# Kernel optimization log

Hardware: AMD Instinct MI355X
Metric: run time of the kernel (lower is better)

## Reference

```python
import jax, jax.numpy as jnp
from jax import lax
import numpy as np

# db4 (Daubechies-4) filters, matching pywt.Wavelet('db4')
L = 8
_REC_LO = np.array([0.23037781330885523, 0.7148465705525415, 0.6308807679295904,
                    -0.02798376941698385, -0.18703481171888114, 0.030841381835986965,
                    0.032883011666982945, -0.010597401784997278], dtype=np.float32)
_DEC_LO = _REC_LO[::-1].copy()
_DEC_HI = (((-1.0) ** (np.arange(L) + 1)) * _REC_LO).astype(np.float32)  # QMF
_REC_HI = _DEC_HI[::-1].copy()
# lax.conv performs correlation, so use reversed filters to get true convolution.
# rev(dec_lo)=rec_lo, rev(dec_hi)=rec_hi and vice versa.
DEC_K = jnp.asarray(np.stack([_DEC_LO[::-1], _DEC_HI[::-1]])[:, None, :])  # (2,1,L)
REC_K = jnp.asarray(np.stack([_REC_LO[::-1], _REC_HI[::-1]])[None, :, :])  # (1,2,L)

ENHANCE_FACTOR = 1.5
DENOISE_THRESHOLD = 0.2


def _dwt_last(x):
    # pywt single-level DWT (mode='symmetric') along last axis.
    # Equivalent to: conv(sym_pad(x, L-1), dec_filter)[valid][1::2]
    xe = jnp.pad(x, ((0, 0), (L - 1, L - 1)), mode='symmetric')[:, 1:]
    y = lax.conv_general_dilated(xe[:, None, :], DEC_K, (2,), 'VALID',
                                 dimension_numbers=('NCH', 'OIH', 'NCH'))
    return y[:, 0], y[:, 1]  # lo, hi, each (M, (S+L-1)//2)


def _idwt_last(lo, hi):
    # pywt single-level IDWT: upsample (lhs_dilation=2), filter, trim L-2 each side.
    c = jnp.stack([lo, hi], axis=1)  # (M, 2, n)
    y = lax.conv_general_dilated(c, REC_K, (1,), [(1, 1)], lhs_dilation=(2,),
                                 dimension_numbers=('NCH', 'OIH', 'NCH'))
    return y[:, 0]  # (M, 2n - L + 2)


def _dwt2(x):
    # x: (N, H, W) -> aa (cA), da (cH), ad (cV), dd (cD)
    N, H, W = x.shape
    lo, hi = _dwt_last(x.reshape(N * H, W))
    Wc = lo.shape[-1]
    lo = lo.reshape(N, H, Wc)
    hi = hi.reshape(N, H, Wc)

    def colwise(a):
        at = a.transpose(0, 2, 1).reshape(N * Wc, H)
        l, h = _dwt_last(at)
        Hc = l.shape[-1]
        return (l.reshape(N, Wc, Hc).transpose(0, 2, 1),
                h.reshape(N, Wc, Hc).transpose(0, 2, 1))

    aa, da = colwise(lo)
    ad, dd = colwise(hi)
    return aa, da, ad, dd


def _idwt2(aa, da, ad, dd):
    N, Hc, Wc = aa.shape

    def colinv(a, d):
        at = a.transpose(0, 2, 1).reshape(N * Wc, Hc)
        dt = d.transpose(0, 2, 1).reshape(N * Wc, Hc)
        r = _idwt_last(at, dt)
        H = r.shape[-1]
        return r.reshape(N, Wc, H).transpose(0, 2, 1)

    lo = colinv(aa, da)
    hi = colinv(ad, dd)
    H = lo.shape[1]
    out = _idwt_last(lo.reshape(N * H, Wc), hi.reshape(N * H, Wc))
    return out.reshape(N, H, -1)


def _soft_enhance(d):
    # enhance then pywt.threshold(..., mode='soft') with per-(image,channel,band) max
    d = d * ENHANCE_FACTOR
    t = DENOISE_THRESHOLD * jnp.max(jnp.abs(d), axis=(-2, -1), keepdims=True)
    return jnp.sign(d) * jnp.maximum(jnp.abs(d) - t, 0.0)


def setup_inputs() -> dict:
    key = jax.random.key(0)
    x = jax.random.normal(key, (32, 3, 510, 510), dtype=jnp.float32)
    return {'x': x}


def reference(x):
    B, C, H, W = x.shape
    z = x.reshape(B * C, H, W)
    a1, h1, v1, d1 = _dwt2(z)
    a2, h2, v2, d2 = _dwt2(a1)
    h2s, v2s, d2s = _soft_enhance(h2), _soft_enhance(v2), _soft_enhance(d2)
    h1s, v1s, d1s = _soft_enhance(h1), _soft_enhance(v1), _soft_enhance(d1)
    a1r = _idwt2(a2, h2s, v2s, d2s)
    out = _idwt2(a1r, h1s, v1s, d1s)
    return out.reshape(B, C, H, W)
```

## Files before the change

### kernel.cpp

```cpp
#include <hip/hip_runtime.h>

__constant__ float c_dec_lo[8] = {
    -0.010597401784997278f, 0.032883011666982945f, 0.030841381835986965f,
    -0.18703481171888114f, -0.02798376941698385f, 0.6308807679295904f,
    0.7148465705525415f, 0.23037781330885523f};
__constant__ float c_dec_hi[8] = {
    -0.23037781330885523f, 0.7148465705525415f, -0.6308807679295904f,
    -0.02798376941698385f, 0.18703481171888114f, 0.030841381835986965f,
    -0.032883011666982945f, -0.010597401784997278f};
__constant__ float c_rec_lo[8] = {
    0.23037781330885523f, 0.7148465705525415f, 0.6308807679295904f,
    -0.02798376941698385f, -0.18703481171888114f, 0.030841381835986965f,
    0.032883011666982945f, -0.010597401784997278f};
__constant__ float c_rec_hi[8] = {
    -0.010597401784997278f, -0.032883011666982945f, 0.030841381835986965f,
    0.18703481171888114f, -0.02798376941698385f, -0.6308807679295904f,
    0.7148465705525415f, -0.23037781330885523f};

__device__ __forceinline__ float soft_enh(float v, float th) {
    float e = 1.5f * v;
    float a = fabsf(e) - th;
    return a > 0.0f ? copysignf(a, e) : 0.0f;
}

#define TB 32
#define TO 64

__global__ __launch_bounds__(256, 8) void fused_dwt2_k(
    const float* __restrict__ x, int S, int Nc, int tiles,
    float* __restrict__ aa, float* __restrict__ da,
    float* __restrict__ ad, float* __restrict__ dd,
    unsigned* __restrict__ mx_da, unsigned* __restrict__ mx_ad,
    unsigned* __restrict__ mx_dd)
{
    int b = blockIdx.x;
    int tx = b % tiles, ty = (b / tiles) % tiles, m = b / (tiles * tiles);
    int jh0 = ty * TB, jw0 = tx * TB;
    int r0 = 2 * jh0 - 6, c0 = 2 * jw0 - 6;
    const float* xm = x + (size_t)m * S * S;

    __shared__ float RB[70][65];

    int tid = threadIdx.x;
    bool interior = (r0 >= 0) & (r0 + 69 < S) & (c0 >= 0) & (c0 + 69 < S);

    if (interior) {
        for (int e = tid; e < 70 * 32; e += 256) {
            int r = e >> 5, jj = e & 31;
            const float* row = xm + (size_t)(r0 + r) * S + (c0 + 2 * jj);
            float alo = 0.f, ahi = 0.f;
#pragma unroll
            for (int t = 0; t < 8; ++t) {
                float v = row[7 - t];
                alo = fmaf(c_dec_lo[t], v, alo);
                ahi = fmaf(c_dec_hi[t], v, ahi);
            }
            RB[r][jj] = alo; RB[r][32 + jj] = ahi;
        }
    } else {
        for (int e = tid; e < 70 * 32; e += 256) {
            int r = e >> 5, jj = e & 31;
            int pr = r0 + r;
            pr = pr < 0 ? -1 - pr : pr;
            pr = pr >= S ? 2 * S - 1 - pr : pr;
            const float* row = xm + (size_t)pr * S;
            int pb = c0 + 2 * jj;
            float alo = 0.f, ahi = 0.f;
#pragma unroll
            for (int t = 0; t < 8; ++t) {
                int p = pb + 7 - t;
                p = p < 0 ? -1 - p : p;
                p = p >= S ? 2 * S - 1 - p : p;
                float v = row[p];
                alo = fmaf(c_dec_lo[t], v, alo);
                ahi = fmaf(c_dec_hi[t], v, ahi);
            }
            RB[r][jj] = alo; RB[r][32 + jj] = ahi;
        }
    }
    __syncthreads();

    float mh = 0.f, mv = 0.f, md = 0.f;
    for (int e = tid; e < TB * TB; e += 256) {
        int ii = e >> 5, jj = e & 31;
        float vaa = 0.f, vda = 0.f, vad = 0.f, vdd = 0.f;
#pragma unroll
        for (int t = 0; t < 8; ++t) {
            float l = RB[2 * ii + 7 - t][jj];
            float h = RB[2 * ii + 7 - t][32 + jj];
            vaa = fmaf(c_dec_lo[t], l, vaa);
            vda = fmaf(c_dec_hi[t], l, vda);
            vad = fmaf(c_dec_lo[t], h, vad);
            vdd = fmaf(c_dec_hi[t], h, vdd);
        }
        int jh = jh0 + ii, jw = jw0 + jj;
        if (jh < Nc && jw < Nc) {
            size_t o = ((size_t)m * Nc + jh) * Nc + jw;
            aa[o] = vaa; da[o] = vda; ad[o] = vad; dd[o] = vdd;
            mh = fmaxf(mh, fabsf(vda));
            mv = fmaxf(mv, fabsf(vad));
            md = fmaxf(md, fabsf(vdd));
        }
    }
#pragma unroll
    for (int off = 32; off; off >>= 1) {
        mh = fmaxf(mh, __shfl_down(mh, off));
        mv = fmaxf(mv, __shfl_down(mv, off));
        md = fmaxf(md, __shfl_down(md, off));
    }
    __shared__ float sm[3][4];
    int wv = tid >> 6, ln = tid & 63;
    if (ln == 0) { sm[0][wv] = mh; sm[1][wv] = mv; sm[2][wv] = md; }
    __syncthreads();
    if (tid == 0) {
        float A = fmaxf(fmaxf(sm[0][0], sm[0][1]), fmaxf(sm[0][2], sm[0][3]));
        float B = fmaxf(fmaxf(sm[1][0], sm[1][1]), fmaxf(sm[1][2], sm[1][3]));
        float C = fmaxf(fmaxf(sm[2][0], sm[2][1]), fmaxf(sm[2][2], sm[2][3]));
        atomicMax(mx_da + m, __float_as_uint(A));
        atomicMax(mx_ad + m, __float_as_uint(B));
        atomicMax(mx_dd + m, __float_as_uint(C));
    }
}

__global__ __launch_bounds__(256, 6) void fused_idwt2_k(
    const float* __restrict__ a, const float* __restrict__ h,
    const float* __restrict__ v, const float* __restrict__ d,
    const unsigned* __restrict__ mxh, const unsigned* __restrict__ mxv,
    const unsigned* __restrict__ mxd,
    int n, int Ho, int tiles, float* __restrict__ out)
{
    int b = blockIdx.x;
    int tx = b % tiles, ty = (b / tiles) % tiles, m = b / (tiles * tiles);
    int i0 = ty * TO, u0 = tx * TO;
    int jr0 = i0 >> 1, jc0 = u0 >> 1;

    __shared__ float LH[TO][71];

    int tid = threadIdx.x;
    float th_h = 0.2f * (1.5f * __uint_as_float(mxh[m]));
    float th_v = 0.2f * (1.5f * __uint_as_float(mxv[m]));
    float th_d = 0.2f * (1.5f * __uint_as_float(mxd[m]));
    const float* am = a + (size_t)m * n * n;
    const float* hm = h + (size_t)m * n * n;
    const float* vm = v + (size_t)m * n * n;
    const float* dm = d + (size_t)m * n * n;

    for (int task = tid; task < 8 * 35; task += 256) {
        int g = task / 35, jc = task % 35;
        int jcg = jc0 + jc; if (jcg > n - 1) jcg = n - 1;
        float acc_lo[8], acc_hi[8];
#pragma unroll
        for (int k = 0; k < 8; ++k) { acc_lo[k] = 0.f; acc_hi[k] = 0.f; }
#pragma unroll
        for (int rl = 0; rl < 7; ++rl) {
            int jr = jr0 + 4 * g + rl; if (jr > n - 1) jr = n - 1;
            size_t o = (size_t)jr * n + jcg;
            float av = am[o];
            float hv = soft_enh(hm[o], th_h);
            float vv = soft_enh(vm[o], th_v);
            float dv = soft_enh(dm[o], th_d);
#pragma unroll
            for (int t = 0; t < 8; ++t) {
                int il = 2 * rl + t - 6;
                if (il >= 0 && il < 8) {
                    acc_lo[il] = fmaf(c_rec_lo[t], av, fmaf(c_rec_hi[t], hv, acc_lo[il]));
                    acc_hi[il] = fmaf(c_rec_lo[t], vv, fmaf(c_rec_hi[t], dv, acc_hi[il]));
                }
            }
        }
#pragma unroll
        for (int k = 0; k < 8; ++k) {
            LH[8 * g + k][jc] = acc_lo[k];
            LH[8 * g + k][35 + jc] = acc_hi[k];
        }
    }
    __syncthreads();

    for (int e = tid; e < TO * TO; e += 256) {
        int il = e >> 6, ul = e & 63;
        int t0 = ul & 1;
        float acc = 0.f;
#pragma unroll
        for (int s = 0; s < 4; ++s) {
            int t = t0 + 2 * s;
            int c = (ul + 6 - t) >> 1;
            acc = fmaf(c_rec_lo[t], LH[il][c], acc);
            acc = fmaf(c_rec_hi[t], LH[il][35 + c], acc);
        }
        int gi = i0 + il, gu = u0 + ul;
        if (gi < Ho && gu < Ho)
            out[((size_t)m * Ho + gi) * Ho + gu] = acc;
    }
}

extern "C" void kernel_launch(void* const* d_in, const int* in_sizes, int n_in,
                              void* d_out, int out_size, void* d_ws, size_t ws_size,
                              hipStream_t stream) {
    const float* x = (const float*)d_in[0];
    float* out = (float*)d_out;
    float* ws = (float*)d_ws;

    const int M = 96, S1 = 510, N1 = 258, N2 = 132;
    const long S_l1 = (long)M * N1 * N1;
    const long S_l2 = (long)M * N2 * N2;

    float* aa1 = ws;
    float* h1  = aa1 + S_l1;
    float* v1  = h1 + S_l1;
    float* d1  = v1 + S_l1;
    float* a1r = d1 + S_l1;
    float* a2  = a1r + S_l1;
    float* h2  = a2 + S_l2;
    float* v2  = h2 + S_l2;
    float* d2  = v2 + S_l2;
    unsigned* th = (unsigned*)(d2 + S_l2);

    long need = 5 * S_l1 + 4 * S_l2 + 576;
    if (ws_size < (size_t)need * sizeof(float)) return;

    unsigned *th_h1 = th, *th_v1 = th + 96, *th_d1 = th + 192;
    unsigned *th_h2 = th + 288, *th_v2 = th + 384, *th_d2 = th + 480;

    hipMemsetAsync(th, 0, 576 * sizeof(unsigned), stream);

    fused_dwt2_k<<<9 * 9 * M, 256, 0, stream>>>(x, S1, N1, 9, aa1, h1, v1, d1,
                                                th_h1, th_v1, th_d1);
    fused_dwt2_k<<<5 * 5 * M, 256, 0, stream>>>(aa1, N1, N2, 5, a2, h2, v2, d2,
                                                th_h2, th_v2, th_d2);
    fused_idwt2_k<<<5 * 5 * M, 256, 0, stream>>>(a2, h2, v2, d2, th_h2, th_v2, th_d2,
                                                 N2, N1, 5, a1r);
    fused_idwt2_k<<<8 * 8 * M, 256, 0, stream>>>(a1r, h1, v1, d1, th_h1, th_v1, th_d1,
                                                 N1, S1, 8, out);
}
```

Measured before the change: 366.6 us.

## Vectorize DWT row loads, register-block column pass, split IDWT row tasks

The forward DWT row pass now uses a column-only interior test. Each thread loads 16 contiguous inputs with float2 loads and produces 4 lo/hi outputs, stored as float4 into a 68-wide padded shared buffer. The column pass gives each thread a fixed column and 4 output rows, loading 10 shared rows into registers and reusing them across outputs instead of re-reading 8 rows per output. The inverse kernel splits each 8-row task into two 4-row passes, which lowers register pressure, and raises launch_bounds occupancy to 8; in exchange it re-reads overlapping input rows from global memory (5 per 4 outputs instead of 7 per 8).

```diff
diff --git a/kernel.cpp b/kernel.cpp
--- a/kernel.cpp
+++ b/kernel.cpp
@@ -39,23 +39,39 @@
     int r0 = 2 * jh0 - 6, c0 = 2 * jw0 - 6;
     const float* xm = x + (size_t)m * S * S;
 
-    __shared__ float RB[70][65];
+    __shared__ float RB[70][68];
 
     int tid = threadIdx.x;
-    bool interior = (r0 >= 0) & (r0 + 69 < S) & (c0 >= 0) & (c0 + 69 < S);
-
-    if (interior) {
-        for (int e = tid; e < 70 * 32; e += 256) {
-            int r = e >> 5, jj = e & 31;
-            const float* row = xm + (size_t)(r0 + r) * S + (c0 + 2 * jj);
-            float alo = 0.f, ahi = 0.f;
-#pragma unroll
-            for (int t = 0; t < 8; ++t) {
-                float v = row[7 - t];
-                alo = fmaf(c_dec_lo[t], v, alo);
-                ahi = fmaf(c_dec_hi[t], v, ahi);
-            }
-            RB[r][jj] = alo; RB[r][32 + jj] = ahi;
+    bool colv = (c0 >= 0) && (c0 + 71 < S);
+
+    if (colv) {
+        for (int e = tid; e < 560; e += 256) {
+            int r = e >> 3, q = e & 7;
+            int pr = r0 + r;
+            pr = pr < 0 ? -1 - pr : pr;
+            pr = pr >= S ? 2 * S - 1 - pr : pr;
+            const float* src = xm + (size_t)pr * S + (c0 + 8 * q);
+            float f[16];
+#pragma unroll
+            for (int i = 0; i < 8; ++i) {
+                float2 v = *reinterpret_cast<const float2*>(src + 2 * i);
+                f[2 * i] = v.x; f[2 * i + 1] = v.y;
+            }
+            float lo[4], hi[4];
+#pragma unroll
+            for (int i = 0; i < 4; ++i) {
+                float alo = 0.f, ahi = 0.f;
+#pragma unroll
+                for (int t = 0; t < 8; ++t) {
+                    float v = f[2 * i + 7 - t];
+                    alo = fmaf(c_dec_lo[t], v, alo);
+                    ahi = fmaf(c_dec_hi[t], v, ahi);
+                }
+                lo[i] = alo; hi[i] = ahi;
+            }
+            int c4 = 4 * q;
+            *reinterpret_cast<float4*>(&RB[r][c4]) = make_float4(lo[0], lo[1], lo[2], lo[3]);
+            *reinterpret_cast<float4*>(&RB[r][32 + c4]) = make_float4(hi[0], hi[1], hi[2], hi[3]);
         }
     } else {
         for (int e = tid; e < 70 * 32; e += 256) {
@@ -80,26 +96,38 @@
     }
     __syncthreads();
 
+    int jj = tid & 31, g = tid >> 5;
+    int jw = jw0 + jj;
     float mh = 0.f, mv = 0.f, md = 0.f;
-    for (int e = tid; e < TB * TB; e += 256) {
-        int ii = e >> 5, jj = e & 31;
-        float vaa = 0.f, vda = 0.f, vad = 0.f, vdd = 0.f;
-#pragma unroll
-        for (int t = 0; t < 8; ++t) {
-            float l = RB[2 * ii + 7 - t][jj];
-            float h = RB[2 * ii + 7 - t][32 + jj];
-            vaa = fmaf(c_dec_lo[t], l, vaa);
-            vda = fmaf(c_dec_hi[t], l, vda);
-            vad = fmaf(c_dec_lo[t], h, vad);
-            vdd = fmaf(c_dec_hi[t], h, vdd);
-        }
-        int jh = jh0 + ii, jw = jw0 + jj;
-        if (jh < Nc && jw < Nc) {
-            size_t o = ((size_t)m * Nc + jh) * Nc + jw;
-            aa[o] = vaa; da[o] = vda; ad[o] = vad; dd[o] = vdd;
-            mh = fmaxf(mh, fabsf(vda));
-            mv = fmaxf(mv, fabsf(vad));
-            md = fmaxf(md, fabsf(vdd));
+#pragma unroll
+    for (int pass = 0; pass < 2; ++pass) {
+        int rbase = 8 * g + 4 * pass;
+        float L[10], H[10];
+#pragma unroll
+        for (int rr = 0; rr < 10; ++rr) {
+            L[rr] = RB[rbase + rr][jj];
+            H[rr] = RB[rbase + rr][32 + jj];
+        }
+#pragma unroll
+        for (int k = 0; k < 2; ++k) {
+            float vaa = 0.f, vda = 0.f, vad = 0.f, vdd = 0.f;
+#pragma unroll
+            for (int t = 0; t < 8; ++t) {
+                float l = L[2 * k + 7 - t];
+                float h = H[2 * k + 7 - t];
+                vaa = fmaf(c_dec_lo[t], l, vaa);
+                vda = fmaf(c_dec_hi[t], l, vda);
+                vad = fmaf(c_dec_lo[t], h, vad);
+                vdd = fmaf(c_dec_hi[t], h, vdd);
+            }
+            int jh = jh0 + 4 * g + 2 * pass + k;
+            if (jh < Nc && jw < Nc) {
+                size_t o = ((size_t)m * Nc + jh) * Nc + jw;
+                aa[o] = vaa; da[o] = vda; ad[o] = vad; dd[o] = vdd;
+                mh = fmaxf(mh, fabsf(vda));
+                mv = fmaxf(mv, fabsf(vad));
+                md = fmaxf(md, fabsf(vdd));
+            }
         }
     }
 #pragma unroll
@@ -122,7 +150,7 @@
     }
 }
 
-__global__ __launch_bounds__(256, 6) void fused_idwt2_k(
+__global__ __launch_bounds__(256, 8) void fused_idwt2_k(
     const float* __restrict__ a, const float* __restrict__ h,
     const float* __restrict__ v, const float* __restrict__ d,
     const unsigned* __restrict__ mxh, const unsigned* __restrict__ mxv,
@@ -148,30 +176,34 @@
     for (int task = tid; task < 8 * 35; task += 256) {
         int g = task / 35, jc = task % 35;
         int jcg = jc0 + jc; if (jcg > n - 1) jcg = n - 1;
-        float acc_lo[8], acc_hi[8];
-#pragma unroll
-        for (int k = 0; k < 8; ++k) { acc_lo[k] = 0.f; acc_hi[k] = 0.f; }
-#pragma unroll
-        for (int rl = 0; rl < 7; ++rl) {
-            int jr = jr0 + 4 * g + rl; if (jr > n - 1) jr = n - 1;
-            size_t o = (size_t)jr * n + jcg;
-            float av = am[o];
-            float hv = soft_enh(hm[o], th_h);
-            float vv = soft_enh(vm[o], th_v);
-            float dv = soft_enh(dm[o], th_d);
-#pragma unroll
-            for (int t = 0; t < 8; ++t) {
-                int il = 2 * rl + t - 6;
-                if (il >= 0 && il < 8) {
-                    acc_lo[il] = fmaf(c_rec_lo[t], av, fmaf(c_rec_hi[t], hv, acc_lo[il]));
-                    acc_hi[il] = fmaf(c_rec_lo[t], vv, fmaf(c_rec_hi[t], dv, acc_hi[il]));
+#pragma unroll
+        for (int pass = 0; pass < 2; ++pass) {
+            int P = 2 * g + pass;
+            float acc_lo[4], acc_hi[4];
+#pragma unroll
+            for (int k = 0; k < 4; ++k) { acc_lo[k] = 0.f; acc_hi[k] = 0.f; }
+#pragma unroll
+            for (int rl = 0; rl < 5; ++rl) {
+                int jr = jr0 + 2 * P + rl; if (jr > n - 1) jr = n - 1;
+                size_t o = (size_t)jr * n + jcg;
+                float av = am[o];
+                float hv = soft_enh(hm[o], th_h);
+                float vv = soft_enh(vm[o], th_v);
+                float dv = soft_enh(dm[o], th_d);
+#pragma unroll
+                for (int t = 0; t < 8; ++t) {
+                    int k = 2 * rl + t - 6;
+                    if (k >= 0 && k < 4) {
+                        acc_lo[k] = fmaf(c_rec_lo[t], av, fmaf(c_rec_hi[t], hv, acc_lo[k]));
+                        acc_hi[k] = fmaf(c_rec_lo[t], vv, fmaf(c_rec_hi[t], dv, acc_hi[k]));
+                    }
                 }
             }
-        }
-#pragma unroll
-        for (int k = 0; k < 8; ++k) {
-            LH[8 * g + k][jc] = acc_lo[k];
-            LH[8 * g + k][35 + jc] = acc_hi[k];
+#pragma unroll
+            for (int k = 0; k < 4; ++k) {
+                LH[4 * P + k][jc] = acc_lo[k];
+                LH[4 * P + k][35 + jc] = acc_hi[k];
+            }
         }
     }
     __syncthreads();
```

Result: faster. 359.0 us (-2.1%).
